# Optimization experiments

Measured on AMD Instinct MI355X. Metric: run time of the kernel, lower is better.

Reference implementation:

```python
import jax, jax.numpy as jnp
import numpy as np

B = 1                 # images
GRID = 30             # patch grid per side (HEIGHT_FACTOR*2)
NIMG = GRID * GRID    # 900 tokens per image
EMBED = 1152
HEADS = 16
DH = EMBED // HEADS   # 72
DHH = DH // 2         # 36
LAYERS = 6
FF = 4608             # mlp intermediate (4*EMBED)
MERGE = 2
MHID = EMBED * MERGE * MERGE   # 4608 merger hidden
OUT = 2048
DS_IDX = (2, 5)
PS = 16               # spatial patch size
TP = 2                # temporal patch size
THETA = 10000.0


def _rope_cos_sin():
    # 2D rotary positions in merge-block order: (Hf, Wf, mh, mw)
    HF = GRID // MERGE
    I, J, MH, MW = np.meshgrid(np.arange(HF), np.arange(HF), np.arange(MERGE), np.arange(MERGE), indexing='ij')
    hpos = (I * MERGE + MH).reshape(-1).astype(np.float32)
    wpos = (J * MERGE + MW).reshape(-1).astype(np.float32)
    inv = 1.0 / (THETA ** (np.arange(0, DHH, 2, dtype=np.float32) / DHH))      # [DH//4]
    rot = np.concatenate([hpos[:, None] * inv, wpos[:, None] * inv], axis=-1)  # [NIMG, DHH]
    cos = np.concatenate([np.cos(rot), np.cos(rot)], axis=-1)[None, None]      # [1,1,NIMG,DH]
    sin = np.concatenate([np.sin(rot), np.sin(rot)], axis=-1)[None, None]
    return jnp.asarray(cos, jnp.float32), jnp.asarray(sin, jnp.float32)


def _ln(x, w, b, eps=1e-6):
    mu = x.mean(-1, keepdims=True)
    xc = x - mu
    v = (xc * xc).mean(-1, keepdims=True)
    return xc * jax.lax.rsqrt(v + eps) * w + b


def _rot_half(t):
    t1, t2 = jnp.split(t, 2, axis=-1)
    return jnp.concatenate([-t2, t1], axis=-1)


def setup_inputs():
    key = jax.random.key(0)
    ks = jax.random.split(key, 12)
    s = 0.02
    n = lambda k, sh: jax.random.normal(k, sh, jnp.float32) * s
    z = lambda sh: jnp.zeros(sh, jnp.float32)
    o = lambda sh: jnp.ones(sh, jnp.float32)
    cos, sin = _rope_cos_sin()
    return {
        'pixel_values': jax.random.uniform(ks[0], (B, 1, 3, GRID * PS, GRID * PS), jnp.float32) * 255.0,
        'patch_w': n(ks[1], (EMBED, 3 * TP * PS * PS)), 'patch_b': z((EMBED,)),
        'pos_emb': n(ks[2], (1, NIMG, EMBED)),
        'cos': cos, 'sin': sin,
        'ln1_w': o((LAYERS, EMBED)), 'ln1_b': z((LAYERS, EMBED)),
        'qkv_w': n(ks[3], (LAYERS, 3 * EMBED, EMBED)), 'qkv_b': z((LAYERS, 3 * EMBED)),
        'proj_w': n(ks[4], (LAYERS, EMBED, EMBED)), 'proj_b': z((LAYERS, EMBED)),
        'ln2_w': o((LAYERS, EMBED)), 'ln2_b': z((LAYERS, EMBED)),
        'fc1_w': n(ks[5], (LAYERS, FF, EMBED)), 'fc1_b': z((LAYERS, FF)),
        'fc2_w': n(ks[6], (LAYERS, EMBED, FF)), 'fc2_b': z((LAYERS, EMBED)),
        'ds_norm_w': o((2, MHID)), 'ds_norm_b': z((2, MHID)),
        'ds_fc1_w': n(ks[7], (2, MHID, MHID)), 'ds_fc1_b': z((2, MHID)),
        'ds_fc2_w': n(ks[8], (2, OUT, MHID)), 'ds_fc2_b': z((2, OUT)),
        'm_norm_w': o((EMBED,)), 'm_norm_b': z((EMBED,)),
        'm_fc1_w': n(ks[9], (MHID, MHID)), 'm_fc1_b': z((MHID,)),
        'm_fc2_w': n(ks[10], (OUT, MHID)), 'm_fc2_b': z((OUT,)),
    }


def _forward(pixel_values, patch_w, patch_b, pos_emb, cos, sin, ln1_w, ln1_b, qkv_w, qkv_b, proj_w, proj_b, ln2_w, ln2_b, fc1_w, fc1_b, fc2_w, fc2_b, ds_norm_w, ds_norm_b, ds_fc1_w, ds_fc1_b, ds_fc2_w, ds_fc2_b, m_norm_w, m_norm_b, m_fc1_w, m_fc1_b, m_fc2_w, m_fc2_b):
    HF = GRID // MERGE
    x = (pixel_values - 127.5) * (1.0 / 127.5)                 # [B,1,3,H,W]
    x = jnp.concatenate([x, x], axis=1)                        # temporal duplication -> [B,2,3,H,W]
    x = x.reshape(B, 1, TP, 3, HF, MERGE, PS, HF, MERGE, PS)
    x = jnp.transpose(x, (0, 1, 4, 7, 5, 8, 3, 2, 6, 9))       # [B,1,HF,WF,mh,mw,3,TP,ps,ps]
    x = x.reshape(-1, 3 * TP * PS * PS)                        # [B*NIMG, 1536] (conv3d == matmul)
    h = (x @ patch_w.T + patch_b).reshape(1, -1, EMBED)        # [1, N, E]
    N = B * NIMG
    h = h + jnp.tile(pos_emb, (1, B, 1))
    cosf = jnp.tile(cos, (1, 1, B, 1))                         # [1,1,N,DH]
    sinf = jnp.tile(sin, (1, 1, B, 1))
    ds = []
    for l in range(LAYERS):
        hn = _ln(h, ln1_w[l], ln1_b[l])
        qkv = (hn @ qkv_w[l].T + qkv_b[l]).reshape(N, 3, HEADS, DH)
        qkv = jnp.transpose(qkv, (1, 2, 0, 3))                 # [3, H, N, dh]
        q, k, v = qkv[0][None], qkv[1][None], qkv[2][None]     # [1, H, N, dh]
        q = q * cosf + _rot_half(q) * sinf                     # inline RoPE (q,k pre-scaled by dh**-0.25 in weights)
        k = k * cosf + _rot_half(k) * sinf
        qb = jnp.transpose(q[0].reshape(HEADS, B, NIMG, DH), (1, 0, 2, 3))  # per-image attention blocks
        kb = jnp.transpose(k[0].reshape(HEADS, B, NIMG, DH), (1, 0, 2, 3))
        vb = jnp.transpose(v[0].reshape(HEADS, B, NIMG, DH), (1, 0, 2, 3))
        attn = jax.nn.softmax(jnp.einsum('bhqd,bhkd->bhqk', qb, kb), axis=-1)
        o = jnp.einsum('bhqk,bhkd->bhqd', attn, vb)            # [B, H, NIMG, dh]
        o = jnp.transpose(o, (0, 2, 1, 3)).reshape(1, N, EMBED)
        h = h + (o @ proj_w[l].T + proj_b[l])
        m = jax.nn.gelu(_ln(h, ln2_w[l], ln2_b[l]) @ fc1_w[l].T + fc1_b[l], approximate=True)
        h = h + (m @ fc2_w[l].T + fc2_b[l])
        if l in DS_IDX:
            d = DS_IDX.index(l)
            xm = _ln(h.reshape(1, -1, MHID), ds_norm_w[d], ds_norm_b[d])
            xm = jax.nn.gelu(xm @ ds_fc1_w[d].T + ds_fc1_b[d], approximate=True) @ ds_fc2_w[d].T + ds_fc2_b[d]
            ds.append(xm)                                      # [1, N/4, OUT]
    hm = _ln(h, m_norm_w, m_norm_b).reshape(1, -1, MHID)
    out = jax.nn.gelu(hm @ m_fc1_w.T + m_fc1_b, approximate=True) @ m_fc2_w.T + m_fc2_b
    return ds, out


def reference(pixel_values, patch_w, patch_b, pos_emb, cos, sin, ln1_w, ln1_b, qkv_w, qkv_b, proj_w, proj_b, ln2_w, ln2_b, fc1_w, fc1_b, fc2_w, fc2_b, ds_norm_w, ds_norm_b, ds_fc1_w, ds_fc1_b, ds_fc2_w, ds_fc2_b, m_norm_w, m_norm_b, m_fc1_w, m_fc1_b, m_fc2_w, m_fc2_b):
    ds, out = _forward(pixel_values, patch_w, patch_b, pos_emb, cos, sin, ln1_w, ln1_b, qkv_w, qkv_b, proj_w, proj_b, ln2_w, ln2_b, fc1_w, fc1_b, fc2_w, fc2_b, ds_norm_w, ds_norm_b, ds_fc1_w, ds_fc1_b, ds_fc2_w, ds_fc2_b, m_norm_w, m_norm_b, m_fc1_w, m_fc1_b, m_fc2_w, m_fc2_b)
    return (*ds, out)
```

## Files before the change

### kernel.cpp

```cpp
#include <hip/hip_runtime.h>
#include <hip/hip_bf16.h>
#include <cstdint>

#define NT   900
#define EMB  1152
#define NH   16
#define DHD  72
#define DHH  36
#define DHP  96
#define KVP  928
#define NL   6
#define FFD  4608
#define MHD  4608
#define OUTD 2048
#define NM   225

typedef __attribute__((ext_vector_type(8))) short short8;
typedef __attribute__((ext_vector_type(4))) float f32x4;

__device__ __forceinline__ ushort f2bf(float f) {
    uint32_t u = __float_as_uint(f);
    uint32_t r = u + 0x7FFF + ((u >> 16) & 1);
    return (ushort)(r >> 16);
}
__device__ __forceinline__ float gelu_f(float x) {
    return 0.5f * x * (1.0f + tanhf(0.7978845608f * (x + 0.044715f * x * x * x)));
}

__device__ __forceinline__ void g2lds16(const ushort* g, ushort* l) {
    __builtin_amdgcn_global_load_lds(
        (const __attribute__((address_space(1))) unsigned int*)g,
        (__attribute__((address_space(3))) unsigned int*)l, 16, 0, 0);
}

__global__ __launch_bounds__(256) void k_cvt(const float* __restrict__ src,
                                             ushort* __restrict__ dst, int n4) {
    int idx = blockIdx.x * 256 + threadIdx.x;
    if (idx >= n4) return;
    const float4 v = *(const float4*)(src + (size_t)idx * 4);
    ushort o[4] = { f2bf(v.x), f2bf(v.y), f2bf(v.z), f2bf(v.w) };
    *(uint2*)(dst + (size_t)idx * 4) = *(const uint2*)o;
}

__global__ __launch_bounds__(256) void k_patch(const float* __restrict__ pix,
                                               ushort* __restrict__ xp) {
    int idx = blockIdx.x * 256 + threadIdx.x;
    if (idx >= NT * 1536) return;
    int t = idx / 1536, f = idx - t * 1536;
    int mw = t & 1, mh = (t >> 1) & 1;
    int tq = t >> 2;
    int jj = tq % 15, ii = tq / 15;
    int pw = f & 15, ph = (f >> 4) & 15, c = f >> 9;
    int Hi = (ii * 2 + mh) * 16 + ph;
    int Wi = (jj * 2 + mw) * 16 + pw;
    float p = pix[((size_t)c * 480 + Hi) * 480 + Wi];
    xp[idx] = f2bf((p - 127.5f) * (1.0f / 127.5f));
}

__global__ __launch_bounds__(256) void k_ln(const float* __restrict__ x,
                                            const float* __restrict__ w,
                                            const float* __restrict__ b,
                                            ushort* __restrict__ y, int C) {
    int row = blockIdx.x;
    int tid = threadIdx.x;
    const float* xr = x + (size_t)row * C;
    float s = 0.f, ss = 0.f;
    for (int c = tid; c < C; c += 256) { float v = xr[c]; s += v; ss += v * v; }
    for (int off = 32; off; off >>= 1) {
        s  += __shfl_down(s,  off, 64);
        ss += __shfl_down(ss, off, 64);
    }
    __shared__ float rs[4], rss[4];
    int wid = tid >> 6, lane = tid & 63;
    if (lane == 0) { rs[wid] = s; rss[wid] = ss; }
    __syncthreads();
    float S  = rs[0] + rs[1] + rs[2] + rs[3];
    float SS = rss[0] + rss[1] + rss[2] + rss[3];
    float mu  = S / C;
    float var = SS / C - mu * mu;
    float inv = rsqrtf(var + 1e-6f);
    ushort* yr = y + (size_t)row * C;
    for (int c = tid; c < C; c += 256) yr[c] = f2bf((xr[c] - mu) * inv * w[c] + b[c]);
}

__global__ __launch_bounds__(256) void k_fixln(const float* __restrict__ part,
                                               const float* __restrict__ bias,
                                               const float* __restrict__ res,
                                               float* __restrict__ hout,
                                               const float* __restrict__ lw,
                                               const float* __restrict__ lb,
                                               ushort* __restrict__ y,
                                               int C, int S, long MN) {
    int row = blockIdx.x, tid = threadIdx.x;
    int C4 = C >> 2;
    const float* prow = part + (size_t)row * C;
    const float* rrow = res + (size_t)row * C;
    float* hrow = hout + (size_t)row * C;
    ushort* yrow = y + (size_t)row * C;

    float4 vals[2];
    float s = 0.f, ss = 0.f;
    int idx[2] = { tid, tid + 256 };
#pragma unroll
    for (int it = 0; it < 2; ++it) {
        int c4 = idx[it];
        if (c4 < C4) {
            float4 v = *(const float4*)(prow + c4 * 4);
            for (int sI = 1; sI < S; ++sI) {
                const float4 p = *(const float4*)(prow + (size_t)sI * MN + c4 * 4);
                v.x += p.x; v.y += p.y; v.z += p.z; v.w += p.w;
            }
            const float4 bi = *(const float4*)(bias + c4 * 4);
            v.x += bi.x; v.y += bi.y; v.z += bi.z; v.w += bi.w;
            const float4 rr = *(const float4*)(rrow + c4 * 4);
            v.x += rr.x; v.y += rr.y; v.z += rr.z; v.w += rr.w;
            *(float4*)(hrow + c4 * 4) = v;
            vals[it] = v;
            s  += v.x + v.y + v.z + v.w;
            ss += v.x * v.x + v.y * v.y + v.z * v.z + v.w * v.w;
        }
    }
    for (int off = 32; off; off >>= 1) {
        s  += __shfl_down(s,  off, 64);
        ss += __shfl_down(ss, off, 64);
    }
    __shared__ float rs[4], rss[4];
    int wid = tid >> 6, lane = tid & 63;
    if (lane == 0) { rs[wid] = s; rss[wid] = ss; }
    __syncthreads();
    float St  = rs[0] + rs[1] + rs[2] + rs[3];
    float SSt = rss[0] + rss[1] + rss[2] + rss[3];
    float mu  = St / C;
    float var = SSt / C - mu * mu;
    float inv = rsqrtf(var + 1e-6f);
#pragma unroll
    for (int it = 0; it < 2; ++it) {
        int c4 = idx[it];
        if (c4 < C4) {
            float4 v = vals[it];
            const float4 w4 = *(const float4*)(lw + c4 * 4);
            const float4 b4 = *(const float4*)(lb + c4 * 4);
            ushort o[4] = { f2bf((v.x - mu) * inv * w4.x + b4.x),
                            f2bf((v.y - mu) * inv * w4.y + b4.y),
                            f2bf((v.z - mu) * inv * w4.z + b4.z),
                            f2bf((v.w - mu) * inv * w4.w + b4.w) };
            *(uint2*)(yrow + c4 * 4) = *(const uint2*)o;
        }
    }
}

template <int ACT, int OBF16, int SPLIT>
__global__ __launch_bounds__(256) void k_bgs(const ushort* __restrict__ A,
                                             const ushort* __restrict__ W,
                                             const float* __restrict__ bias,
                                             const float* __restrict__ res,
                                             void* __restrict__ Cp,
                                             float* __restrict__ part,
                                             int M, int N, int K, int S) {
    __shared__ __align__(16) ushort As[64 * 64];
    __shared__ __align__(16) ushort Bs[64 * 64];
    int tid = threadIdx.x;
    int row0 = blockIdx.x * 64, col0 = blockIdx.y * 64;
    int z = blockIdx.z;
    int Kc = K / S;
    int kbeg = z * Kc;
    int steps = Kc >> 6;

    int w = tid >> 6, lane = tid & 63;
    int lrow = lane >> 3;
    int cg   = ((lane & 7) ^ lrow) << 3;

    int ar0 = row0 + w * 16 + lrow; if (ar0 > M - 1) ar0 = M - 1;
    int ar1 = row0 + w * 16 + 8 + lrow; if (ar1 > M - 1) ar1 = M - 1;
    int wr0 = col0 + w * 16 + lrow;
    int wr1 = wr0 + 8;
    const ushort* ap0 = A + (size_t)ar0 * K + kbeg + cg;
    const ushort* ap1 = A + (size_t)ar1 * K + kbeg + cg;
    const ushort* wp0 = W + (size_t)wr0 * K + kbeg + cg;
    const ushort* wp1 = W + (size_t)wr1 * K + kbeg + cg;
    ushort* asd0 = &As[(w * 16) * 64];
    ushort* asd1 = &As[(w * 16 + 8) * 64];
    ushort* bsd0 = &Bs[(w * 16) * 64];
    ushort* bsd1 = &Bs[(w * 16 + 8) * 64];

    int fr = lane & 15, kg8 = (lane >> 4) << 3;
    int wrr = (w >> 1) * 32, wcc = (w & 1) * 32;
    int sw = (fr & 7) << 3;

    f32x4 acc[2][2] = {};
    for (int s = 0; s < steps; ++s) {
        int kk = s << 6;
        __syncthreads();
        g2lds16(ap0 + kk, asd0);
        g2lds16(ap1 + kk, asd1);
        g2lds16(wp0 + kk, bsd0);
        g2lds16(wp1 + kk, bsd1);
        __syncthreads();
#pragma unroll
        for (int j = 0; j < 2; ++j) {
            int ko = j * 32 + kg8;
            int kx = ko ^ sw;
            short8 a0 = *(const short8*)&As[(wrr + fr) * 64 + kx];
            short8 a1 = *(const short8*)&As[(wrr + 16 + fr) * 64 + kx];
            short8 b0 = *(const short8*)&Bs[(wcc + fr) * 64 + kx];
            short8 b1 = *(const short8*)&Bs[(wcc + 16 + fr) * 64 + kx];
            acc[0][0] = __builtin_amdgcn_mfma_f32_16x16x32_bf16(a0, b0, acc[0][0], 0, 0, 0);
            acc[0][1] = __builtin_amdgcn_mfma_f32_16x16x32_bf16(a0, b1, acc[0][1], 0, 0, 0);
            acc[1][0] = __builtin_amdgcn_mfma_f32_16x16x32_bf16(a1, b0, acc[1][0], 0, 0, 0);
            acc[1][1] = __builtin_amdgcn_mfma_f32_16x16x32_bf16(a1, b1, acc[1][1], 0, 0, 0);
        }
    }

#pragma unroll
    for (int fi = 0; fi < 2; fi++)
#pragma unroll
        for (int fj = 0; fj < 2; fj++)
#pragma unroll
            for (int r = 0; r < 4; r++) {
                int row = row0 + wrr + fi * 16 + (lane >> 4) * 4 + r;
                int col = col0 + wcc + fj * 16 + fr;
                if (row < M) {
                    if (SPLIT) {
                        part[((size_t)z * M + row) * N + col] = acc[fi][fj][r];
                    } else {
                        float v = acc[fi][fj][r] + bias[col];
                        if (res) v += res[(size_t)row * N + col];
                        if (ACT == 1) v = gelu_f(v);
                        if (OBF16) ((ushort*)Cp)[(size_t)row * N + col] = f2bf(v);
                        else       ((float*)Cp)[(size_t)row * N + col] = v;
                    }
                }
            }
}

template <int ACT, int OBF16>
__global__ __launch_bounds__(256) void k_fix(const float* __restrict__ part,
                                             const float* __restrict__ bias,
                                             const float* __restrict__ res,
                                             void* __restrict__ Cp,
                                             int M, int N, int S) {
    size_t idx = (size_t)blockIdx.x * 256 + threadIdx.x;
    size_t total = (size_t)M * N / 4;
    if (idx >= total) return;
    size_t e = idx * 4;
    int row = (int)(e / N), col = (int)(e - (size_t)row * N);
    float4 v = *(const float4*)(part + e);
    for (int s = 1; s < S; ++s) {
        const float4 p = *(const float4*)(part + (size_t)s * M * N + e);
        v.x += p.x; v.y += p.y; v.z += p.z; v.w += p.w;
    }
    const float4 bi = *(const float4*)(bias + col);
    v.x += bi.x; v.y += bi.y; v.z += bi.z; v.w += bi.w;
    if (res) {
        const float4 rr = *(const float4*)(res + e);
        v.x += rr.x; v.y += rr.y; v.z += rr.z; v.w += rr.w;
    }
    if (ACT == 1) { v.x = gelu_f(v.x); v.y = gelu_f(v.y); v.z = gelu_f(v.z); v.w = gelu_f(v.w); }
    if (OBF16) {
        ushort o[4] = { f2bf(v.x), f2bf(v.y), f2bf(v.z), f2bf(v.w) };
        *(uint2*)((ushort*)Cp + e) = *(const uint2*)o;
    } else {
        *(float4*)((float*)Cp + e) = v;
    }
}

template <int OBF16>
__global__ __launch_bounds__(256) void k_mm(const ushort* __restrict__ A,
                                            const ushort* __restrict__ Wb,
                                            void* __restrict__ Cp,
                                            int M, int N, int K, int ldc, int Nw,
                                            long as_, long ws_, long cs_) {
    __shared__ __align__(16) ushort As[64 * 40];
    __shared__ __align__(16) ushort Bs[64 * 40];
    int z = blockIdx.z;
    A  += (size_t)z * as_;
    Wb += (size_t)z * ws_;
    float*  Cf = (float*)Cp + (size_t)z * cs_;
    ushort* Cb = (ushort*)Cp + (size_t)z * cs_;

    int tid = threadIdx.x;
    int row0 = blockIdx.y * 64, col0 = blockIdx.x * 64;

    int sm = tid >> 2, sp = tid & 3;
    int ar = row0 + sm; if (ar > M - 1) ar = M - 1;
    int wr = col0 + sm; if (wr > N - 1) wr = N - 1;
    const ushort* aptr = A + (size_t)ar * K;

    int lane = tid & 63, wid = tid >> 6;
    int wrr = (wid >> 1) * 32, wcc = (wid & 1) * 32;
    int fr = lane & 15, kg = lane >> 4;

    f32x4 acc[2][2] = {};

    for (int k0 = 0; k0 < K; k0 += 32) {
        *(uint4*)&As[sm * 40 + sp * 8] = *(const uint4*)(aptr + k0 + sp * 8);
        *(uint4*)&Bs[sm * 40 + sp * 8] = *(const uint4*)(Wb + (size_t)wr * K + k0 + sp * 8);
        __syncthreads();
        short8 a0 = *(const short8*)&As[(wrr + fr) * 40 + kg * 8];
        short8 a1 = *(const short8*)&As[(wrr + 16 + fr) * 40 + kg * 8];
        short8 b0 = *(const short8*)&Bs[(wcc + fr) * 40 + kg * 8];
        short8 b1 = *(const short8*)&Bs[(wcc + 16 + fr) * 40 + kg * 8];
        acc[0][0] = __builtin_amdgcn_mfma_f32_16x16x32_bf16(a0, b0, acc[0][0], 0, 0, 0);
        acc[0][1] = __builtin_amdgcn_mfma_f32_16x16x32_bf16(a0, b1, acc[0][1], 0, 0, 0);
        acc[1][0] = __builtin_amdgcn_mfma_f32_16x16x32_bf16(a1, b0, acc[1][0], 0, 0, 0);
        acc[1][1] = __builtin_amdgcn_mfma_f32_16x16x32_bf16(a1, b1, acc[1][1], 0, 0, 0);
        __syncthreads();
    }

#pragma unroll
    for (int fi = 0; fi < 2; fi++)
#pragma unroll
        for (int fj = 0; fj < 2; fj++)
#pragma unroll
            for (int r = 0; r < 4; r++) {
                int row = row0 + wrr + fi * 16 + (lane >> 4) * 4 + r;
                int col = col0 + wcc + fj * 16 + (lane & 15);
                if (row < M && col < Nw) {
                    float v = acc[fi][fj][r];
                    if (OBF16) Cb[(size_t)row * ldc + col] = f2bf(v);
                    else       Cf[(size_t)row * ldc + col] = v;
                }
            }
}

__global__ __launch_bounds__(256) void k_rope(const float* __restrict__ qkv,
                                              const float* __restrict__ cs,
                                              const float* __restrict__ sn,
                                              ushort* __restrict__ q,
                                              ushort* __restrict__ k,
                                              ushort* __restrict__ vt) {
    int idx = blockIdx.x * 256 + threadIdx.x;
    if (idx >= NT * NH * DHP) return;
    int t = idx / (NH * DHP);
    int rem = idx - t * (NH * DHP);
    int h = rem / DHP, d = rem - h * DHP;
    size_t oi = ((size_t)h * NT + t) * DHP + d;
    if (d < DHD) {
        const float* base = qkv + (size_t)t * 3 * EMB;
        float c = cs[t * DHD + d], s = sn[t * DHD + d];
        int   d2 = (d < DHH) ? d + DHH : d - DHH;
        float sg = (d < DHH) ? -1.f : 1.f;
        int e = h * DHD + d;
        float qv = base[e] * c + sg * base[h * DHD + d2] * s;
        float kv = base[EMB + e] * c + sg * base[EMB + h * DHD + d2] * s;
        q[oi] = f2bf(qv);
        k[oi] = f2bf(kv);
        vt[((size_t)h * DHP + d) * KVP + t] = f2bf(base[2 * EMB + e]);
    } else {
        q[oi] = 0;
        k[oi] = 0;
    }
}

__global__ __launch_bounds__(256) void k_vpad(ushort* __restrict__ vt) {
    int idx = blockIdx.x * 256 + threadIdx.x;
    int tot = NH * DHP * (KVP - NT);
    if (idx >= tot) return;
    int pw = KVP - NT;
    int hd = idx / pw, j = idx - hd * pw;
    vt[(size_t)hd * KVP + NT + j] = 0;
}

__global__ __launch_bounds__(256) void k_sm(const float* __restrict__ S,
                                            ushort* __restrict__ P) {
    int row = blockIdx.x * 4 + (threadIdx.x >> 6);
    int lane = threadIdx.x & 63;
    const float* sp = S + (size_t)row * KVP;
    ushort* pp = P + (size_t)row * KVP;
    float v[15];
#pragma unroll
    for (int i = 0; i < 15; i++) {
        int kt = lane + i * 64;
        v[i] = (kt < NT) ? sp[kt] : -1e30f;
    }
    float mx = -1e30f;
#pragma unroll
    for (int i = 0; i < 15; i++) mx = fmaxf(mx, v[i]);
    for (int off = 32; off; off >>= 1) mx = fmaxf(mx, __shfl_xor(mx, off, 64));
    float sum = 0.f;
#pragma unroll
    for (int i = 0; i < 15; i++) {
        int kt = lane + i * 64;
        v[i] = (kt < NT) ? __expf(v[i] - mx) : 0.f;
        sum += v[i];
    }
    for (int off = 32; off; off >>= 1) sum += __shfl_xor(sum, off, 64);
    float inv = 1.f / sum;
#pragma unroll
    for (int i = 0; i < 15; i++) {
        int kt = lane + i * 64;
        if (kt < KVP) pp[kt] = f2bf(v[i] * inv);
    }
}

extern "C" void kernel_launch(void* const* d_in, const int* in_sizes, int n_in,
                              void* d_out, int out_size, void* d_ws, size_t ws_size,
                              hipStream_t stream) {
    const float* pix     = (const float*)d_in[0];
    const float* patch_w = (const float*)d_in[1];
    const float* patch_b = (const float*)d_in[2];
    const float* pos_emb = (const float*)d_in[3];
    const float* cosb    = (const float*)d_in[4];
    const float* sinb    = (const float*)d_in[5];
    const float* ln1_w   = (const float*)d_in[6];
    const float* ln1_b   = (const float*)d_in[7];
    const float* qkv_w   = (const float*)d_in[8];
    const float* qkv_b   = (const float*)d_in[9];
    const float* proj_w  = (const float*)d_in[10];
    const float* proj_b  = (const float*)d_in[11];
    const float* ln2_w   = (const float*)d_in[12];
    const float* ln2_b   = (const float*)d_in[13];
    const float* fc1_w   = (const float*)d_in[14];
    const float* fc1_b   = (const float*)d_in[15];
    const float* fc2_w   = (const float*)d_in[16];
    const float* fc2_b   = (const float*)d_in[17];
    const float* dsn_w   = (const float*)d_in[18];
    const float* dsn_b   = (const float*)d_in[19];
    const float* ds1_w   = (const float*)d_in[20];
    const float* ds1_b   = (const float*)d_in[21];
    const float* ds2_w   = (const float*)d_in[22];
    const float* ds2_b   = (const float*)d_in[23];
    const float* mn_w    = (const float*)d_in[24];
    const float* mn_b    = (const float*)d_in[25];
    const float* mf1_w   = (const float*)d_in[26];
    const float* mf1_b   = (const float*)d_in[27];
    const float* mf2_w   = (const float*)d_in[28];
    const float* mf2_b   = (const float*)d_in[29];
    float* out = (float*)d_out;

    float* wsf = (float*)d_ws;
    size_t off = 0;
    auto af = [&](size_t n) { float* p = wsf + off; off += (n + 3) & ~(size_t)3; return p; };
    float* h    = af((size_t)NT * EMB);
    float* qkv  = af((size_t)NT * 3 * EMB);
    float* part = af((size_t)4 * NT * EMB);
    float* S    = af((size_t)NH * NT * KVP);
    ushort* wsh = (ushort*)(wsf + off);
    size_t hoff = 0;
    auto ah = [&](size_t n) { ushort* p = wsh + hoff; hoff += (n + 7) & ~(size_t)7; return p; };
    ushort* hn  = ah((size_t)NT * EMB);
    ushort* hn2 = ah((size_t)NM * MHD);
    ushort* qb  = ah((size_t)NH * NT * DHP);
    ushort* kb  = ah((size_t)NH * NT * DHP);
    ushort* vt  = ah((size_t)NH * DHP * KVP);
    ushort* P   = ah((size_t)NH * NT * KVP);
    ushort* ob  = ah((size_t)NT * EMB);
    ushort* t1  = ah((size_t)NT * FFD);
    ushort* xp  = t1;
    ushort* w_patch = ah((size_t)EMB * 1536);
    ushort* w_qkv   = ah((size_t)NL * 3 * EMB * EMB);
    ushort* w_proj  = ah((size_t)NL * EMB * EMB);
    ushort* w_fc1   = ah((size_t)NL * FFD * EMB);
    ushort* w_fc2   = ah((size_t)NL * EMB * FFD);
    ushort* w_ds1   = ah((size_t)2 * MHD * MHD);
    ushort* w_ds2   = ah((size_t)2 * OUTD * MHD);
    ushort* w_mf1   = ah((size_t)MHD * MHD);
    ushort* w_mf2   = ah((size_t)OUTD * MHD);

    const long QS = (long)NT * DHP;
    const long VS = (long)DHP * KVP;
    const long SS = (long)NT * KVP;
    const long MN = (long)NT * EMB;

    const int MB  = (NT + 63) / 64;
    const int MBm = (NM + 63) / 64;
    auto fixg = [](int M, int N) { return dim3(((size_t)M * N / 4 + 255) / 256); };
    auto cvt = [&](const float* s, ushort* d, size_t n) {
        k_cvt<<<dim3((unsigned)((n / 4 + 255) / 256)), 256, 0, stream>>>(s, d, (int)(n / 4));
    };

    cvt(patch_w, w_patch, (size_t)EMB * 1536);
    cvt(qkv_w,   w_qkv,   (size_t)NL * 3 * EMB * EMB);
    cvt(proj_w,  w_proj,  (size_t)NL * EMB * EMB);
    cvt(fc1_w,   w_fc1,   (size_t)NL * FFD * EMB);
    cvt(fc2_w,   w_fc2,   (size_t)NL * EMB * FFD);
    cvt(ds1_w,   w_ds1,   (size_t)2 * MHD * MHD);
    cvt(ds2_w,   w_ds2,   (size_t)2 * OUTD * MHD);
    cvt(mf1_w,   w_mf1,   (size_t)MHD * MHD);
    cvt(mf2_w,   w_mf2,   (size_t)OUTD * MHD);

    k_patch<<<dim3((NT * 1536 + 255) / 256), 256, 0, stream>>>(pix, xp);
    k_vpad<<<dim3((NH * DHP * (KVP - NT) + 255) / 256), 256, 0, stream>>>(vt);
    k_bgs<0, 0, 1><<<dim3(MB, EMB / 64, 2), 256, 0, stream>>>(
        xp, w_patch, nullptr, nullptr, nullptr, part, NT, EMB, 1536, 2);
    k_fixln<<<NT, 256, 0, stream>>>(part, patch_b, pos_emb, h,
                                    ln1_w, ln1_b, hn, EMB, 2, MN);

    for (int l = 0; l < NL; ++l) {
        k_bgs<0, 0, 0><<<dim3(MB, 3 * EMB / 64, 1), 256, 0, stream>>>(
            hn, w_qkv + (size_t)l * 3 * EMB * EMB, qkv_b + l * 3 * EMB, nullptr, qkv,
            nullptr, NT, 3 * EMB, EMB, 1);
        k_rope<<<dim3((NT * NH * DHP + 255) / 256), 256, 0, stream>>>(
            qkv, cosb, sinb, qb, kb, vt);
        k_mm<0><<<dim3(MB, MB, NH), 256, 0, stream>>>(
            qb, kb, S, NT, NT, DHP, KVP, NT, QS, QS, SS);
        k_sm<<<dim3(NH * NT / 4), 256, 0, stream>>>(S, P);
        k_mm<1><<<dim3(2, MB, NH), 256, 0, stream>>>(
            P, vt, ob, NT, DHD, KVP, EMB, DHD, SS, VS, DHD);
        k_bgs<0, 0, 1><<<dim3(MB, EMB / 64, 3), 256, 0, stream>>>(
            ob, w_proj + (size_t)l * EMB * EMB, nullptr, nullptr, nullptr, part,
            NT, EMB, EMB, 3);
        k_fixln<<<NT, 256, 0, stream>>>(part, proj_b + l * EMB, h, h,
                                        ln2_w + l * EMB, ln2_b + l * EMB, hn,
                                        EMB, 3, MN);
        k_bgs<1, 1, 0><<<dim3(MB, FFD / 64, 1), 256, 0, stream>>>(
            hn, w_fc1 + (size_t)l * FFD * EMB, fc1_b + l * FFD, nullptr, t1,
            nullptr, NT, FFD, EMB, 1);
        const float* nlw = (l == NL - 1) ? mn_w : ln1_w + (l + 1) * EMB;
        const float* nlb = (l == NL - 1) ? mn_b : ln1_b + (l + 1) * EMB;
        k_bgs<0, 0, 1><<<dim3(MB, EMB / 64, 4), 256, 0, stream>>>(
            t1, w_fc2 + (size_t)l * EMB * FFD, nullptr, nullptr, nullptr, part,
            NT, EMB, FFD, 4);
        k_fixln<<<NT, 256, 0, stream>>>(part, fc2_b + l * EMB, h, h,
                                        nlw, nlb, hn, EMB, 4, MN);
        if (l == 2 || l == 5) {
            int d = (l == 2) ? 0 : 1;
            k_ln<<<NM, 256, 0, stream>>>(h, dsn_w + d * MHD, dsn_b + d * MHD, hn2, MHD);
            k_bgs<0, 0, 1><<<dim3(MBm, MHD / 64, 4), 256, 0, stream>>>(
                hn2, w_ds1 + (size_t)d * MHD * MHD, nullptr, nullptr, nullptr, part,
                NM, MHD, MHD, 4);
            k_fix<1, 1><<<fixg(NM, MHD), 256, 0, stream>>>(part, ds1_b + d * MHD,
                                                           nullptr, t1, NM, MHD, 4);
            k_bgs<0, 0, 1><<<dim3(MBm, OUTD / 64, 4), 256, 0, stream>>>(
                t1, w_ds2 + (size_t)d * OUTD * MHD, nullptr, nullptr, nullptr, part,
                NM, OUTD, MHD, 4);
            k_fix<0, 0><<<fixg(NM, OUTD), 256, 0, stream>>>(
                part, ds2_b + d * OUTD, nullptr, out + (size_t)d * NM * OUTD,
                NM, OUTD, 4);
        }
    }
    k_bgs<0, 0, 1><<<dim3(MBm, MHD / 64, 4), 256, 0, stream>>>(
        hn, w_mf1, nullptr, nullptr, nullptr, part, NM, MHD, MHD, 4);
    k_fix<1, 1><<<fixg(NM, MHD), 256, 0, stream>>>(part, mf1_b, nullptr, t1, NM, MHD, 4);
    k_bgs<0, 0, 1><<<dim3(MBm, OUTD / 64, 4), 256, 0, stream>>>(
        t1, w_mf2, nullptr, nullptr, nullptr, part, NM, OUTD, MHD, 4);
    k_fix<0, 0><<<fixg(NM, OUTD), 256, 0, stream>>>(
        part, mf2_b, nullptr, out + (size_t)2 * NM * OUTD, NM, OUTD, 4);
}
```

Before: 1.442 ms.

## Enlarge GEMM tiles to 128x128 per block and rebalance split-K factors

Replaces the 64x64-tile bf16 MFMA GEMM with a 128x128-tile variant where each wave computes a 64x64 sub-tile with 16 accumulators, raising data reuse from LDS. Because fewer blocks result, split-K factors are increased across GEMMs (and QKV now uses split-K with a separate reduce pass) to keep enough parallelism, with the partials buffer doubled. Trades more register pressure, lower occupancy and extra partial-sum traffic for fewer global/LDS loads per FLOP.

```diff
diff --git a/kernel.cpp b/kernel.cpp
--- a/kernel.cpp
+++ b/kernel.cpp
@@ -149,18 +149,40 @@
     }
 }
 
+#define RD_A(i) (*(const short8*)&As[(wro + 16*(i) + fr) * 64 + kx])
+#define RD_B(i) (*(const short8*)&Bs[(wco + 16*(i) + fr) * 64 + kx])
+#define EPI(CV, I, JJ)                                                          \
+    do {                                                                        \
+        _Pragma("unroll")                                                       \
+        for (int r = 0; r < 4; ++r) {                                           \
+            int row = row0 + wro + (I) * 16 + (lane >> 4) * 4 + r;              \
+            int col = col0 + wco + (JJ) * 16 + fr;                              \
+            if (row < M) {                                                      \
+                if (SPLIT) {                                                    \
+                    part[((size_t)z * M + row) * N + col] = CV[r];              \
+                } else {                                                        \
+                    float v = CV[r] + bias[col];                                \
+                    if (res) v += res[(size_t)row * N + col];                   \
+                    if (ACT == 1) v = gelu_f(v);                                \
+                    if (OBF16) ((ushort*)Cp)[(size_t)row * N + col] = f2bf(v);  \
+                    else       ((float*)Cp)[(size_t)row * N + col] = v;         \
+                }                                                               \
+            }                                                                   \
+        }                                                                       \
+    } while (0)
+
 template <int ACT, int OBF16, int SPLIT>
-__global__ __launch_bounds__(256) void k_bgs(const ushort* __restrict__ A,
-                                             const ushort* __restrict__ W,
-                                             const float* __restrict__ bias,
-                                             const float* __restrict__ res,
-                                             void* __restrict__ Cp,
-                                             float* __restrict__ part,
-                                             int M, int N, int K, int S) {
-    __shared__ __align__(16) ushort As[64 * 64];
-    __shared__ __align__(16) ushort Bs[64 * 64];
+__global__ __launch_bounds__(256) void k_b2(const ushort* __restrict__ A,
+                                            const ushort* __restrict__ W,
+                                            const float* __restrict__ bias,
+                                            const float* __restrict__ res,
+                                            void* __restrict__ Cp,
+                                            float* __restrict__ part,
+                                            int M, int N, int K, int S) {
+    __shared__ __align__(16) ushort As[128 * 64];
+    __shared__ __align__(16) ushort Bs[128 * 64];
     int tid = threadIdx.x;
-    int row0 = blockIdx.x * 64, col0 = blockIdx.y * 64;
+    int row0 = blockIdx.x * 128, col0 = blockIdx.y * 128;
     int z = blockIdx.z;
     int Kc = K / S;
     int kbeg = z * Kc;
@@ -170,67 +192,74 @@
     int lrow = lane >> 3;
     int cg   = ((lane & 7) ^ lrow) << 3;
 
-    int ar0 = row0 + w * 16 + lrow; if (ar0 > M - 1) ar0 = M - 1;
-    int ar1 = row0 + w * 16 + 8 + lrow; if (ar1 > M - 1) ar1 = M - 1;
-    int wr0 = col0 + w * 16 + lrow;
-    int wr1 = wr0 + 8;
-    const ushort* ap0 = A + (size_t)ar0 * K + kbeg + cg;
-    const ushort* ap1 = A + (size_t)ar1 * K + kbeg + cg;
-    const ushort* wp0 = W + (size_t)wr0 * K + kbeg + cg;
-    const ushort* wp1 = W + (size_t)wr1 * K + kbeg + cg;
-    ushort* asd0 = &As[(w * 16) * 64];
-    ushort* asd1 = &As[(w * 16 + 8) * 64];
-    ushort* bsd0 = &Bs[(w * 16) * 64];
-    ushort* bsd1 = &Bs[(w * 16 + 8) * 64];
+    int ra0 = row0 + w * 32 + lrow;
+    int a0r = ra0;      if (a0r > M - 1) a0r = M - 1;
+    int a1r = ra0 + 8;  if (a1r > M - 1) a1r = M - 1;
+    int a2r = ra0 + 16; if (a2r > M - 1) a2r = M - 1;
+    int a3r = ra0 + 24; if (a3r > M - 1) a3r = M - 1;
+    int wb = col0 + w * 32 + lrow;
+    const ushort* ap0 = A + (size_t)a0r * K + kbeg + cg;
+    const ushort* ap1 = A + (size_t)a1r * K + kbeg + cg;
+    const ushort* ap2 = A + (size_t)a2r * K + kbeg + cg;
+    const ushort* ap3 = A + (size_t)a3r * K + kbeg + cg;
+    const ushort* wp0 = W + (size_t)wb * K + kbeg + cg;
+    const ushort* wp1 = W + (size_t)(wb + 8) * K + kbeg + cg;
+    const ushort* wp2 = W + (size_t)(wb + 16) * K + kbeg + cg;
+    const ushort* wp3 = W + (size_t)(wb + 24) * K + kbeg + cg;
+    ushort* la0 = &As[(w * 32) * 64];
+    ushort* la1 = &As[(w * 32 + 8) * 64];
+    ushort* la2 = &As[(w * 32 + 16) * 64];
+    ushort* la3 = &As[(w * 32 + 24) * 64];
+    ushort* lb0 = &Bs[(w * 32) * 64];
+    ushort* lb1 = &Bs[(w * 32 + 8) * 64];
+    ushort* lb2 = &Bs[(w * 32 + 16) * 64];
+    ushort* lb3 = &Bs[(w * 32 + 24) * 64];
 
     int fr = lane & 15, kg8 = (lane >> 4) << 3;
-    int wrr = (w >> 1) * 32, wcc = (w & 1) * 32;
+    int wro = (w >> 1) * 64, wco = (w & 1) * 64;
     int sw = (fr & 7) << 3;
 
-    f32x4 acc[2][2] = {};
+    f32x4 c00 = {}, c01 = {}, c02 = {}, c03 = {};
+    f32x4 c10 = {}, c11 = {}, c12 = {}, c13 = {};
+    f32x4 c20 = {}, c21 = {}, c22 = {}, c23 = {};
+    f32x4 c30 = {}, c31 = {}, c32 = {}, c33 = {};
+
     for (int s = 0; s < steps; ++s) {
         int kk = s << 6;
         __syncthreads();
-        g2lds16(ap0 + kk, asd0);
-        g2lds16(ap1 + kk, asd1);
-        g2lds16(wp0 + kk, bsd0);
-        g2lds16(wp1 + kk, bsd1);
+        g2lds16(ap0 + kk, la0); g2lds16(ap1 + kk, la1);
+        g2lds16(ap2 + kk, la2); g2lds16(ap3 + kk, la3);
+        g2lds16(wp0 + kk, lb0); g2lds16(wp1 + kk, lb1);
+        g2lds16(wp2 + kk, lb2); g2lds16(wp3 + kk, lb3);
         __syncthreads();
 #pragma unroll
         for (int j = 0; j < 2; ++j) {
-            int ko = j * 32 + kg8;
-            int kx = ko ^ sw;
-            short8 a0 = *(const short8*)&As[(wrr + fr) * 64 + kx];
-            short8 a1 = *(const short8*)&As[(wrr + 16 + fr) * 64 + kx];
-            short8 b0 = *(const short8*)&Bs[(wcc + fr) * 64 + kx];
-            short8 b1 = *(const short8*)&Bs[(wcc + 16 + fr) * 64 + kx];
-            acc[0][0] = __builtin_amdgcn_mfma_f32_16x16x32_bf16(a0, b0, acc[0][0], 0, 0, 0);
-            acc[0][1] = __builtin_amdgcn_mfma_f32_16x16x32_bf16(a0, b1, acc[0][1], 0, 0, 0);
-            acc[1][0] = __builtin_amdgcn_mfma_f32_16x16x32_bf16(a1, b0, acc[1][0], 0, 0, 0);
-            acc[1][1] = __builtin_amdgcn_mfma_f32_16x16x32_bf16(a1, b1, acc[1][1], 0, 0, 0);
+            int kx = (j * 32 + kg8) ^ sw;
+            short8 a0 = RD_A(0), a1 = RD_A(1), a2 = RD_A(2), a3 = RD_A(3);
+            short8 b0 = RD_B(0), b1 = RD_B(1), b2 = RD_B(2), b3 = RD_B(3);
+            c00 = __builtin_amdgcn_mfma_f32_16x16x32_bf16(a0, b0, c00, 0, 0, 0);
+            c01 = __builtin_amdgcn_mfma_f32_16x16x32_bf16(a0, b1, c01, 0, 0, 0);
+            c02 = __builtin_amdgcn_mfma_f32_16x16x32_bf16(a0, b2, c02, 0, 0, 0);
+            c03 = __builtin_amdgcn_mfma_f32_16x16x32_bf16(a0, b3, c03, 0, 0, 0);
+            c10 = __builtin_amdgcn_mfma_f32_16x16x32_bf16(a1, b0, c10, 0, 0, 0);
+            c11 = __builtin_amdgcn_mfma_f32_16x16x32_bf16(a1, b1, c11, 0, 0, 0);
+            c12 = __builtin_amdgcn_mfma_f32_16x16x32_bf16(a1, b2, c12, 0, 0, 0);
+            c13 = __builtin_amdgcn_mfma_f32_16x16x32_bf16(a1, b3, c13, 0, 0, 0);
+            c20 = __builtin_amdgcn_mfma_f32_16x16x32_bf16(a2, b0, c20, 0, 0, 0);
+            c21 = __builtin_amdgcn_mfma_f32_16x16x32_bf16(a2, b1, c21, 0, 0, 0);
+            c22 = __builtin_amdgcn_mfma_f32_16x16x32_bf16(a2, b2, c22, 0, 0, 0);
+            c23 = __builtin_amdgcn_mfma_f32_16x16x32_bf16(a2, b3, c23, 0, 0, 0);
+            c30 = __builtin_amdgcn_mfma_f32_16x16x32_bf16(a3, b0, c30, 0, 0, 0);
+            c31 = __builtin_amdgcn_mfma_f32_16x16x32_bf16(a3, b1, c31, 0, 0, 0);
+            c32 = __builtin_amdgcn_mfma_f32_16x16x32_bf16(a3, b2, c32, 0, 0, 0);
+            c33 = __builtin_amdgcn_mfma_f32_16x16x32_bf16(a3, b3, c33, 0, 0, 0);
         }
     }
 
-#pragma unroll
-    for (int fi = 0; fi < 2; fi++)
-#pragma unroll
-        for (int fj = 0; fj < 2; fj++)
-#pragma unroll
-            for (int r = 0; r < 4; r++) {
-                int row = row0 + wrr + fi * 16 + (lane >> 4) * 4 + r;
-                int col = col0 + wcc + fj * 16 + fr;
-                if (row < M) {
-                    if (SPLIT) {
-                        part[((size_t)z * M + row) * N + col] = acc[fi][fj][r];
-                    } else {
-                        float v = acc[fi][fj][r] + bias[col];
-                        if (res) v += res[(size_t)row * N + col];
-                        if (ACT == 1) v = gelu_f(v);
-                        if (OBF16) ((ushort*)Cp)[(size_t)row * N + col] = f2bf(v);
-                        else       ((float*)Cp)[(size_t)row * N + col] = v;
-                    }
-                }
-            }
+    EPI(c00, 0, 0); EPI(c01, 0, 1); EPI(c02, 0, 2); EPI(c03, 0, 3);
+    EPI(c10, 1, 0); EPI(c11, 1, 1); EPI(c12, 1, 2); EPI(c13, 1, 3);
+    EPI(c20, 2, 0); EPI(c21, 2, 1); EPI(c22, 2, 2); EPI(c23, 2, 3);
+    EPI(c30, 3, 0); EPI(c31, 3, 1); EPI(c32, 3, 2); EPI(c33, 3, 3);
 }
 
 template <int ACT, int OBF16>
@@ -433,7 +462,7 @@
     auto af = [&](size_t n) { float* p = wsf + off; off += (n + 3) & ~(size_t)3; return p; };
     float* h    = af((size_t)NT * EMB);
     float* qkv  = af((size_t)NT * 3 * EMB);
-    float* part = af((size_t)4 * NT * EMB);
+    float* part = af((size_t)8 * NT * EMB);
     float* S    = af((size_t)NH * NT * KVP);
     ushort* wsh = (ushort*)(wsf + off);
     size_t hoff = 0;
@@ -462,8 +491,9 @@
     const long SS = (long)NT * KVP;
     const long MN = (long)NT * EMB;
 
-    const int MB  = (NT + 63) / 64;
-    const int MBm = (NM + 63) / 64;
+    const int MB2  = (NT + 127) / 128;
+    const int MBm2 = (NM + 127) / 128;
+    const int MBa  = (NT + 63) / 64;
     auto fixg = [](int M, int N) { return dim3(((size_t)M * N / 4 + 255) / 256); };
     auto cvt = [&](const float* s, ushort* d, size_t n) {
         k_cvt<<<dim3((unsigned)((n / 4 + 255) / 256)), 256, 0, stream>>>(s, d, (int)(n / 4));
@@ -481,34 +511,36 @@
 
     k_patch<<<dim3((NT * 1536 + 255) / 256), 256, 0, stream>>>(pix, xp);
     k_vpad<<<dim3((NH * DHP * (KVP - NT) + 255) / 256), 256, 0, stream>>>(vt);
-    k_bgs<0, 0, 1><<<dim3(MB, EMB / 64, 2), 256, 0, stream>>>(
-        xp, w_patch, nullptr, nullptr, nullptr, part, NT, EMB, 1536, 2);
+    k_b2<0, 0, 1><<<dim3(MB2, EMB / 128, 6), 256, 0, stream>>>(
+        xp, w_patch, nullptr, nullptr, nullptr, part, NT, EMB, 1536, 6);
     k_fixln<<<NT, 256, 0, stream>>>(part, patch_b, pos_emb, h,
-                                    ln1_w, ln1_b, hn, EMB, 2, MN);
+                                    ln1_w, ln1_b, hn, EMB, 6, MN);
 
     for (int l = 0; l < NL; ++l) {
-        k_bgs<0, 0, 0><<<dim3(MB, 3 * EMB / 64, 1), 256, 0, stream>>>(
-            hn, w_qkv + (size_t)l * 3 * EMB * EMB, qkv_b + l * 3 * EMB, nullptr, qkv,
-            nullptr, NT, 3 * EMB, EMB, 1);
+        k_b2<0, 0, 1><<<dim3(MB2, 3 * EMB / 128, 2), 256, 0, stream>>>(
+            hn, w_qkv + (size_t)l * 3 * EMB * EMB, nullptr, nullptr, nullptr, part,
+            NT, 3 * EMB, EMB, 2);
+        k_fix<0, 0><<<fixg(NT, 3 * EMB), 256, 0, stream>>>(
+            part, qkv_b + l * 3 * EMB, nullptr, qkv, NT, 3 * EMB, 2);
         k_rope<<<dim3((NT * NH * DHP + 255) / 256), 256, 0, stream>>>(
             qkv, cosb, sinb, qb, kb, vt);
-        k_mm<0><<<dim3(MB, MB, NH), 256, 0, stream>>>(
+        k_mm<0><<<dim3(MBa, MBa, NH), 256, 0, stream>>>(
             qb, kb, S, NT, NT, DHP, KVP, NT, QS, QS, SS);
         k_sm<<<dim3(NH * NT / 4), 256, 0, stream>>>(S, P);
-        k_mm<1><<<dim3(2, MB, NH), 256, 0, stream>>>(
+        k_mm<1><<<dim3(2, MBa, NH), 256, 0, stream>>>(
             P, vt, ob, NT, DHD, KVP, EMB, DHD, SS, VS, DHD);
-        k_bgs<0, 0, 1><<<dim3(MB, EMB / 64, 3), 256, 0, stream>>>(
+        k_b2<0, 0, 1><<<dim3(MB2, EMB / 128, 6), 256, 0, stream>>>(
             ob, w_proj + (size_t)l * EMB * EMB, nullptr, nullptr, nullptr, part,
-            NT, EMB, EMB, 3);
+            NT, EMB, EMB, 6);
         k_fixln<<<NT, 256, 0, stream>>>(part, proj_b + l * EMB, h, h,
                                         ln2_w + l * EMB, ln2_b + l * EMB, hn,
-                                        EMB, 3, MN);
-        k_bgs<1, 1, 0><<<dim3(MB, FFD / 64, 1), 256, 0, stream>>>(
+                                        EMB, 6, MN);
+        k_b2<1, 1, 0><<<dim3(MB2, FFD / 128, 1), 256, 0, stream>>>(
             hn, w_fc1 + (size_t)l * FFD * EMB, fc1_b + l * FFD, nullptr, t1,
             nullptr, NT, FFD, EMB, 1);
         const float* nlw = (l == NL - 1) ? mn_w : ln1_w + (l + 1) * EMB;
         const float* nlb = (l == NL - 1) ? mn_b : ln1_b + (l + 1) * EMB;
-        k_bgs<0, 0, 1><<<dim3(MB, EMB / 64, 4), 256, 0, stream>>>(
+        k_b2<0, 0, 1><<<dim3(MB2, EMB / 128, 4), 256, 0, stream>>>(
             t1, w_fc2 + (size_t)l * EMB * FFD, nullptr, nullptr, nullptr, part,
             NT, EMB, FFD, 4);
         k_fixln<<<NT, 256, 0, stream>>>(part, fc2_b + l * EMB, h, h,
@@ -516,24 +548,24 @@
         if (l == 2 || l == 5) {
             int d = (l == 2) ? 0 : 1;
             k_ln<<<NM, 256, 0, stream>>>(h, dsn_w + d * MHD, dsn_b + d * MHD, hn2, MHD);
-            k_bgs<0, 0, 1><<<dim3(MBm, MHD / 64, 4), 256, 0, stream>>>(
+            k_b2<0, 0, 1><<<dim3(MBm2, MHD / 128, 8), 256, 0, stream>>>(
                 hn2, w_ds1 + (size_t)d * MHD * MHD, nullptr, nullptr, nullptr, part,
-                NM, MHD, MHD, 4);
+                NM, MHD, MHD, 8);
             k_fix<1, 1><<<fixg(NM, MHD), 256, 0, stream>>>(part, ds1_b + d * MHD,
-                                                           nullptr, t1, NM, MHD, 4);
-            k_bgs<0, 0, 1><<<dim3(MBm, OUTD / 64, 4), 256, 0, stream>>>(
+                                                           nullptr, t1, NM, MHD, 8);
+            k_b2<0, 0, 1><<<dim3(MBm2, OUTD / 128, 12), 256, 0, stream>>>(
                 t1, w_ds2 + (size_t)d * OUTD * MHD, nullptr, nullptr, nullptr, part,
-                NM, OUTD, MHD, 4);
+                NM, OUTD, MHD, 12);
             k_fix<0, 0><<<fixg(NM, OUTD), 256, 0, stream>>>(
                 part, ds2_b + d * OUTD, nullptr, out + (size_t)d * NM * OUTD,
-                NM, OUTD, 4);
+                NM, OUTD, 12);
         }
     }
-    k_bgs<0, 0, 1><<<dim3(MBm, MHD / 64, 4), 256, 0, stream>>>(
-        hn, w_mf1, nullptr, nullptr, nullptr, part, NM, MHD, MHD, 4);
-    k_fix<1, 1><<<fixg(NM, MHD), 256, 0, stream>>>(part, mf1_b, nullptr, t1, NM, MHD, 4);
-    k_bgs<0, 0, 1><<<dim3(MBm, OUTD / 64, 4), 256, 0, stream>>>(
-        t1, w_mf2, nullptr, nullptr, nullptr, part, NM, OUTD, MHD, 4);
+    k_b2<0, 0, 1><<<dim3(MBm2, MHD / 128, 8), 256, 0, stream>>>(
+        hn, w_mf1, nullptr, nullptr, nullptr, part, NM, MHD, MHD, 8);
+    k_fix<1, 1><<<fixg(NM, MHD), 256, 0, stream>>>(part, mf1_b, nullptr, t1, NM, MHD, 8);
+    k_b2<0, 0, 1><<<dim3(MBm2, OUTD / 128, 12), 256, 0, stream>>>(
+        t1, w_mf2, nullptr, nullptr, nullptr, part, NM, OUTD, MHD, 12);
     k_fix<0, 0><<<fixg(NM, OUTD), 256, 0, stream>>>(
-        part, mf2_b, nullptr, out + (size_t)2 * NM * OUTD, NM, OUTD, 4);
-}
+        part, mf2_b, nullptr, out + (size_t)2 * NM * OUTD, NM, OUTD, 12);
+}
```

Measured after the change: 1.626 ms. +12.8%, slower.

## Replace unfused QK/softmax/PV attention with split-KV flash attention plus combine

Applied to the files above, without the earlier changes.

Replaces the three-kernel attention path (QK^T matmul to fp32 scores, row softmax to bf16 probabilities, PV matmul) with a flash-attention kernel. It keeps scores in registers and LDS, applies online softmax, and splits the KV sequence into 4 chunks over grid z. A small combine kernel merges the per-split partial outputs and (max, sum) statistics. This removes the large score and probability round-trips through global memory and adds one extra pass over the partial outputs. Softmax scale is not applied, matching the original, which also did not apply it.

```diff
diff --git a/kernel.cpp b/kernel.cpp
--- a/kernel.cpp
+++ b/kernel.cpp
@@ -262,65 +262,6 @@
     } else {
         *(float4*)((float*)Cp + e) = v;
     }
-}
-
-template <int OBF16>
-__global__ __launch_bounds__(256) void k_mm(const ushort* __restrict__ A,
-                                            const ushort* __restrict__ Wb,
-                                            void* __restrict__ Cp,
-                                            int M, int N, int K, int ldc, int Nw,
-                                            long as_, long ws_, long cs_) {
-    __shared__ __align__(16) ushort As[64 * 40];
-    __shared__ __align__(16) ushort Bs[64 * 40];
-    int z = blockIdx.z;
-    A  += (size_t)z * as_;
-    Wb += (size_t)z * ws_;
-    float*  Cf = (float*)Cp + (size_t)z * cs_;
-    ushort* Cb = (ushort*)Cp + (size_t)z * cs_;
-
-    int tid = threadIdx.x;
-    int row0 = blockIdx.y * 64, col0 = blockIdx.x * 64;
-
-    int sm = tid >> 2, sp = tid & 3;
-    int ar = row0 + sm; if (ar > M - 1) ar = M - 1;
-    int wr = col0 + sm; if (wr > N - 1) wr = N - 1;
-    const ushort* aptr = A + (size_t)ar * K;
-
-    int lane = tid & 63, wid = tid >> 6;
-    int wrr = (wid >> 1) * 32, wcc = (wid & 1) * 32;
-    int fr = lane & 15, kg = lane >> 4;
-
-    f32x4 acc[2][2] = {};
-
-    for (int k0 = 0; k0 < K; k0 += 32) {
-        *(uint4*)&As[sm * 40 + sp * 8] = *(const uint4*)(aptr + k0 + sp * 8);
-        *(uint4*)&Bs[sm * 40 + sp * 8] = *(const uint4*)(Wb + (size_t)wr * K + k0 + sp * 8);
-        __syncthreads();
-        short8 a0 = *(const short8*)&As[(wrr + fr) * 40 + kg * 8];
-        short8 a1 = *(const short8*)&As[(wrr + 16 + fr) * 40 + kg * 8];
-        short8 b0 = *(const short8*)&Bs[(wcc + fr) * 40 + kg * 8];
-        short8 b1 = *(const short8*)&Bs[(wcc + 16 + fr) * 40 + kg * 8];
-        acc[0][0] = __builtin_amdgcn_mfma_f32_16x16x32_bf16(a0, b0, acc[0][0], 0, 0, 0);
-        acc[0][1] = __builtin_amdgcn_mfma_f32_16x16x32_bf16(a0, b1, acc[0][1], 0, 0, 0);
-        acc[1][0] = __builtin_amdgcn_mfma_f32_16x16x32_bf16(a1, b0, acc[1][0], 0, 0, 0);
-        acc[1][1] = __builtin_amdgcn_mfma_f32_16x16x32_bf16(a1, b1, acc[1][1], 0, 0, 0);
-        __syncthreads();
-    }
-
-#pragma unroll
-    for (int fi = 0; fi < 2; fi++)
-#pragma unroll
-        for (int fj = 0; fj < 2; fj++)
-#pragma unroll
-            for (int r = 0; r < 4; r++) {
-                int row = row0 + wrr + fi * 16 + (lane >> 4) * 4 + r;
-                int col = col0 + wcc + fj * 16 + (lane & 15);
-                if (row < M && col < Nw) {
-                    float v = acc[fi][fj][r];
-                    if (OBF16) Cb[(size_t)row * ldc + col] = f2bf(v);
-                    else       Cf[(size_t)row * ldc + col] = v;
-                }
-            }
 }
 
 __global__ __launch_bounds__(256) void k_rope(const float* __restrict__ qkv,
@@ -361,36 +302,181 @@
     vt[(size_t)hd * KVP + NT + j] = 0;
 }
 
-__global__ __launch_bounds__(256) void k_sm(const float* __restrict__ S,
-                                            ushort* __restrict__ P) {
-    int row = blockIdx.x * 4 + (threadIdx.x >> 6);
-    int lane = threadIdx.x & 63;
-    const float* sp = S + (size_t)row * KVP;
-    ushort* pp = P + (size_t)row * KVP;
-    float v[15];
-#pragma unroll
-    for (int i = 0; i < 15; i++) {
-        int kt = lane + i * 64;
-        v[i] = (kt < NT) ? sp[kt] : -1e30f;
-    }
-    float mx = -1e30f;
-#pragma unroll
-    for (int i = 0; i < 15; i++) mx = fmaxf(mx, v[i]);
-    for (int off = 32; off; off >>= 1) mx = fmaxf(mx, __shfl_xor(mx, off, 64));
-    float sum = 0.f;
-#pragma unroll
-    for (int i = 0; i < 15; i++) {
-        int kt = lane + i * 64;
-        v[i] = (kt < NT) ? __expf(v[i] - mx) : 0.f;
-        sum += v[i];
-    }
-    for (int off = 32; off; off >>= 1) sum += __shfl_xor(sum, off, 64);
-    float inv = 1.f / sum;
-#pragma unroll
-    for (int i = 0; i < 15; i++) {
-        int kt = lane + i * 64;
-        if (kt < KVP) pp[kt] = f2bf(v[i] * inv);
-    }
+__global__ __launch_bounds__(256) void k_fa2(const ushort* __restrict__ qg,
+                                             const ushort* __restrict__ kg,
+                                             const ushort* __restrict__ vg,
+                                             float* __restrict__ Op,
+                                             float* __restrict__ ml) {
+    __shared__ __align__(16) ushort Qs[64 * 104];
+    __shared__ __align__(16) ushort Ks[64 * 104];
+    __shared__ __align__(16) ushort Vs[80 * 76];
+    __shared__ __align__(16) ushort Ps[4][16 * 76];
+
+    const int h  = blockIdx.y;
+    const int q0 = blockIdx.x * 64;
+    const int z  = blockIdx.z;
+    const int s0 = z * 4;
+    const int s1 = (z == 3) ? 15 : s0 + 4;
+    const int tid = threadIdx.x;
+    const int lane = tid & 63, w = tid >> 6;
+    const int fr = lane & 15, g = lane >> 4;
+
+    const ushort* qh = qg + (size_t)h * (NT * DHP);
+    const ushort* kh = kg + (size_t)h * (NT * DHP);
+    const ushort* vh = vg + (size_t)h * (DHP * KVP);
+
+    for (int i = tid; i < 768; i += 256) {
+        int row = i / 12, cj = i % 12;
+        int gr = q0 + row; if (gr > NT - 1) gr = NT - 1;
+        *(uint4*)&Qs[row * 104 + cj * 8] = *(const uint4*)(qh + (size_t)gr * DHP + cj * 8);
+    }
+    __syncthreads();
+    short8 aq[3];
+#pragma unroll
+    for (int ks = 0; ks < 3; ++ks)
+        aq[ks] = *(const short8*)&Qs[(w * 16 + fr) * 104 + ks * 32 + g * 8];
+
+    uint4 rk[3], rv[3];
+    auto loadKV = [&](int s) {
+        int k0 = s * 64;
+#pragma unroll
+        for (int j = 0; j < 3; ++j) {
+            int i = tid + j * 256;
+            int row = i / 12, cj = i % 12;
+            int gr = k0 + row; if (gr > NT - 1) gr = NT - 1;
+            rk[j] = *(const uint4*)(kh + (size_t)gr * DHP + cj * 8);
+        }
+#pragma unroll
+        for (int j = 0; j < 3; ++j) {
+            int i = tid + j * 256;
+            if (i < 640) {
+                int row = i >> 3, cj = i & 7;
+                int gc = k0 + cj * 8; if (gc > KVP - 8) gc = KVP - 8;
+                rv[j] = *(const uint4*)(vh + (size_t)row * KVP + gc);
+            }
+        }
+    };
+    auto writeKV = [&]() {
+#pragma unroll
+        for (int j = 0; j < 3; ++j) {
+            int i = tid + j * 256;
+            int row = i / 12, cj = i % 12;
+            *(uint4*)&Ks[row * 104 + cj * 8] = rk[j];
+        }
+#pragma unroll
+        for (int j = 0; j < 3; ++j) {
+            int i = tid + j * 256;
+            if (i < 640) {
+                int row = i >> 3, cj = i & 7;
+                *(uint4*)&Vs[row * 76 + cj * 8] = rv[j];
+            }
+        }
+    };
+
+    float m[4] = { -1e30f, -1e30f, -1e30f, -1e30f };
+    float lsum[4] = {};
+    f32x4 o[5] = {};
+    ushort* pw = &Ps[w][0];
+
+    loadKV(s0);
+    for (int s = s0; s < s1; ++s) {
+        __syncthreads();
+        writeKV();
+        if (s + 1 < s1) loadKV(s + 1);
+        __syncthreads();
+        f32x4 sc[4] = {};
+#pragma unroll
+        for (int nt = 0; nt < 4; ++nt)
+#pragma unroll
+            for (int ks = 0; ks < 3; ++ks) {
+                short8 b = *(const short8*)&Ks[(nt * 16 + fr) * 104 + ks * 32 + g * 8];
+                sc[nt] = __builtin_amdgcn_mfma_f32_16x16x32_bf16(aq[ks], b, sc[nt], 0, 0, 0);
+            }
+        int kbase = s * 64;
+        if (kbase + 64 > NT) {
+#pragma unroll
+            for (int nt = 0; nt < 4; ++nt)
+                if (kbase + nt * 16 + fr >= NT) {
+                    sc[nt][0] = -1e30f; sc[nt][1] = -1e30f;
+                    sc[nt][2] = -1e30f; sc[nt][3] = -1e30f;
+                }
+        }
+#pragma unroll
+        for (int r = 0; r < 4; ++r) {
+            float tm = fmaxf(fmaxf(sc[0][r], sc[1][r]), fmaxf(sc[2][r], sc[3][r]));
+#pragma unroll
+            for (int off = 1; off < 16; off <<= 1) tm = fmaxf(tm, __shfl_xor(tm, off, 64));
+            float mn = fmaxf(m[r], tm);
+            float scale = __expf(m[r] - mn);
+            m[r] = mn;
+            float ps = 0.f;
+#pragma unroll
+            for (int nt = 0; nt < 4; ++nt) {
+                float p = __expf(sc[nt][r] - mn);
+                ps += p;
+                pw[(g * 4 + r) * 76 + nt * 16 + fr] = f2bf(p);
+            }
+#pragma unroll
+            for (int off = 1; off < 16; off <<= 1) ps += __shfl_xor(ps, off, 64);
+            lsum[r] = lsum[r] * scale + ps;
+#pragma unroll
+            for (int dt = 0; dt < 5; ++dt) o[dt][r] *= scale;
+        }
+#pragma unroll
+        for (int kt = 0; kt < 2; ++kt) {
+            short8 a = *(const short8*)&pw[fr * 76 + kt * 32 + g * 8];
+#pragma unroll
+            for (int dt = 0; dt < 5; ++dt) {
+                short8 b = *(const short8*)&Vs[(dt * 16 + fr) * 76 + kt * 32 + g * 8];
+                o[dt] = __builtin_amdgcn_mfma_f32_16x16x32_bf16(a, b, o[dt], 0, 0, 0);
+            }
+        }
+    }
+#pragma unroll
+    for (int r = 0; r < 4; ++r) {
+        int q = q0 + w * 16 + g * 4 + r;
+        if (fr == 0 && q < NT) {
+            size_t mi = (((size_t)z * NH + h) * NT + q) * 2;
+            ml[mi]     = m[r];
+            ml[mi + 1] = lsum[r];
+        }
+    }
+#pragma unroll
+    for (int dt = 0; dt < 5; ++dt)
+#pragma unroll
+        for (int r = 0; r < 4; ++r) {
+            int q = q0 + w * 16 + g * 4 + r;
+            int d = dt * 16 + fr;
+            if (q < NT)
+                Op[(((size_t)z * NH + h) * NT + q) * 80 + d] = o[dt][r];
+        }
+}
+
+__global__ __launch_bounds__(256) void k_cmb(const float* __restrict__ Op,
+                                             const float* __restrict__ ml,
+                                             ushort* __restrict__ ob) {
+    int idx = blockIdx.x * 256 + threadIdx.x;
+    if (idx >= NH * NT * DHD) return;
+    int h = idx / (NT * DHD);
+    int rem = idx - h * NT * DHD;
+    int q = rem / DHD, d = rem - q * DHD;
+    float mz[4], lz[4];
+    float M = -1e30f;
+#pragma unroll
+    for (int z = 0; z < 4; ++z) {
+        size_t mi = (((size_t)z * NH + h) * NT + q) * 2;
+        mz[z] = ml[mi];
+        lz[z] = ml[mi + 1];
+        M = fmaxf(M, mz[z]);
+    }
+    float L = 0.f, O = 0.f;
+#pragma unroll
+    for (int z = 0; z < 4; ++z) {
+        float wz = __expf(mz[z] - M);
+        L += lz[z] * wz;
+        O += Op[(((size_t)z * NH + h) * NT + q) * 80 + d] * wz;
+    }
+    ob[(size_t)q * EMB + h * DHD + d] = f2bf(O / L);
 }
 
 extern "C" void kernel_launch(void* const* d_in, const int* in_sizes, int n_in,
@@ -435,6 +521,8 @@
     float* qkv  = af((size_t)NT * 3 * EMB);
     float* part = af((size_t)4 * NT * EMB);
     float* S    = af((size_t)NH * NT * KVP);
+    float* Op   = S;
+    float* ml   = S + (size_t)4 * NH * NT * 80;
     ushort* wsh = (ushort*)(wsf + off);
     size_t hoff = 0;
     auto ah = [&](size_t n) { ushort* p = wsh + hoff; hoff += (n + 7) & ~(size_t)7; return p; };
@@ -443,7 +531,6 @@
     ushort* qb  = ah((size_t)NH * NT * DHP);
     ushort* kb  = ah((size_t)NH * NT * DHP);
     ushort* vt  = ah((size_t)NH * DHP * KVP);
-    ushort* P   = ah((size_t)NH * NT * KVP);
     ushort* ob  = ah((size_t)NT * EMB);
     ushort* t1  = ah((size_t)NT * FFD);
     ushort* xp  = t1;
@@ -457,9 +544,6 @@
     ushort* w_mf1   = ah((size_t)MHD * MHD);
     ushort* w_mf2   = ah((size_t)OUTD * MHD);
 
-    const long QS = (long)NT * DHP;
-    const long VS = (long)DHP * KVP;
-    const long SS = (long)NT * KVP;
     const long MN = (long)NT * EMB;
 
     const int MB  = (NT + 63) / 64;
@@ -492,11 +576,8 @@
             nullptr, NT, 3 * EMB, EMB, 1);
         k_rope<<<dim3((NT * NH * DHP + 255) / 256), 256, 0, stream>>>(
             qkv, cosb, sinb, qb, kb, vt);
-        k_mm<0><<<dim3(MB, MB, NH), 256, 0, stream>>>(
-            qb, kb, S, NT, NT, DHP, KVP, NT, QS, QS, SS);
-        k_sm<<<dim3(NH * NT / 4), 256, 0, stream>>>(S, P);
-        k_mm<1><<<dim3(2, MB, NH), 256, 0, stream>>>(
-            P, vt, ob, NT, DHD, KVP, EMB, DHD, SS, VS, DHD);
+        k_fa2<<<dim3(MB, NH, 4), 256, 0, stream>>>(qb, kb, vt, Op, ml);
+        k_cmb<<<dim3((NH * NT * DHD + 255) / 256), 256, 0, stream>>>(Op, ml, ob);
         k_bgs<0, 0, 1><<<dim3(MB, EMB / 64, 3), 256, 0, stream>>>(
             ob, w_proj + (size_t)l * EMB * EMB, nullptr, nullptr, nullptr, part,
             NT, EMB, EMB, 3);
```

Result: no change. 1.463 ms (+1.5%).
